# Kernel optimization log

Hardware: AMD Instinct MI355X
Metric: run time of the kernel (lower is better)

Reference implementation:

```python
import jax, jax.numpy as jnp
import numpy as np

HIDDEN = 1024
BATCH = 16
SEQ = 2048
NEG_INF = -1000000000.0


def setup_inputs() -> dict:
    key = jax.random.key(0)
    k1, k2, k3, k4, k5, k6, k7 = jax.random.split(key, 7)
    scale = 1.0 / np.sqrt(HIDDEN)
    return {
        "query": jax.random.normal(k1, (BATCH, HIDDEN), dtype=jnp.float32),
        "keys": jax.random.normal(k2, (BATCH, SEQ, HIDDEN), dtype=jnp.float32),
        "values": jax.random.normal(k3, (BATCH, SEQ, HIDDEN), dtype=jnp.float32),
        "mask": jax.random.randint(k4, (BATCH, SEQ), 0, 2, dtype=jnp.int32),
        # Learned params (nn.Linear(in, out) weight has shape (out, in); we store transposed for x @ W)
        "W1": jax.random.uniform(k5, (HIDDEN, HIDDEN), dtype=jnp.float32, minval=-scale, maxval=scale),
        "W2": jax.random.uniform(k6, (HIDDEN, HIDDEN), dtype=jnp.float32, minval=-scale, maxval=scale),
        "v": jax.random.uniform(k7, (HIDDEN,), dtype=jnp.float32, minval=-scale, maxval=scale),
    }


def reference(query, keys, values, mask, W1, W2, v):
    # scores = v^T tanh(W1 q + W2 k)
    q_proj = query @ W1                       # (b, h)
    k_proj = jnp.einsum('bsh,hd->bsd', keys, W2)  # (b, s, h)
    scores = jnp.einsum('bsh,h->bs', jnp.tanh(q_proj[:, None, :] + k_proj), v)  # (b, s)
    scores = jnp.where(mask == 0, NEG_INF, scores)
    attention_weights = jax.nn.softmax(scores, axis=1)  # (b, s)
    context = jnp.einsum('bs,bsh->bh', attention_weights, values)  # (b, h)
    return context, attention_weights
```

## Files before the change

kernel.cpp:

```cpp
#include <hip/hip_runtime.h>
#include <hip/hip_bf16.h>
#include <cstdint>
#include <cstddef>

#define HIDDEN 1024
#define BATCH 16
#define SEQ 2048
#define M_TOTAL (BATCH*SEQ)
#define NEG_INF -1000000000.0f

typedef unsigned short u16;
typedef __bf16 bf16x8 __attribute__((ext_vector_type(8)));
typedef unsigned short u16x8 __attribute__((ext_vector_type(8)));
typedef unsigned short u16x4 __attribute__((ext_vector_type(4)));
typedef float f32x4 __attribute__((ext_vector_type(4)));

typedef const __attribute__((address_space(1))) void* gas_ptr;
typedef __attribute__((address_space(3))) void* las_ptr;

__device__ __forceinline__ u16 f2bf(float f) {
    unsigned int x = __float_as_uint(f);
    unsigned int r = (x + 0x7fffu + ((x >> 16) & 1u)) >> 16;
    return (u16)r;
}

__device__ __forceinline__ float fast_tanh(float x) {
    float e = __expf(2.0f * x);
    return 1.0f - 2.0f / (e + 1.0f);
}

__global__ __launch_bounds__(256) void qproj_kernel(
    const float* __restrict__ q, const float* __restrict__ W1,
    float* __restrict__ qp)
{
    const int b  = blockIdx.y;
    const int tl = threadIdx.x & 63;
    const int kc = threadIdx.x >> 6;
    const int n  = blockIdx.x * 64 + tl;
    __shared__ float red[4][64];

    const float* qrow = q + b * HIDDEN;
    float acc = 0.f;
    #pragma unroll 8
    for (int k = kc * 256; k < kc * 256 + 256; ++k)
        acc += qrow[k] * W1[(size_t)k * HIDDEN + n];
    red[kc][tl] = acc;
    __syncthreads();
    if (kc == 0)
        qp[b * HIDDEN + n] = red[0][tl] + red[1][tl] + red[2][tl] + red[3][tl];
}

__global__ __launch_bounds__(256) void w2t_kernel(
    const float* __restrict__ W2, u16* __restrict__ W2T)
{
    __shared__ float tile[64][65];
    const int n0 = blockIdx.x * 64, k0 = blockIdx.y * 64;
    const int tid = threadIdx.x;
    const int c = tid & 63, rb = tid >> 6;
    #pragma unroll
    for (int i = 0; i < 16; ++i) {
        int r = rb + i * 4;
        tile[r][c] = W2[(size_t)(k0 + r) * HIDDEN + n0 + c];
    }
    __syncthreads();
    #pragma unroll
    for (int i = 0; i < 16; ++i) {
        int r = rb + i * 4;
        W2T[(size_t)(n0 + r) * HIDDEN + k0 + c] = f2bf(tile[c][r]);
    }
}

__global__ __launch_bounds__(256) void conv_kernel(
    const float* __restrict__ in, u16* __restrict__ out)
{
    int i = blockIdx.x * 256 + threadIdx.x;
    float4 f = ((const float4*)in)[i];
    u16x4 p;
    p[0] = f2bf(f.x); p[1] = f2bf(f.y); p[2] = f2bf(f.z); p[3] = f2bf(f.w);
    ((u16x4*)out)[i] = p;
}

#define BM 128
#define BN 128
#define BK 64

__global__ __launch_bounds__(256) void scores_v2_kernel(
    const u16*   __restrict__ keysb,
    const u16*   __restrict__ W2T,
    const float* __restrict__ qp,
    const float* __restrict__ v,
    float*       __restrict__ part)
{
    __shared__ __align__(16) u16 Alds[BM * BK];
    __shared__ __align__(16) u16 Blds[BN * BK];

    const int tid  = threadIdx.x;
    const int nt   = blockIdx.x;
    const int n0   = nt * BN;
    const int m0   = blockIdx.y * BM;
    const int wave = tid >> 6, lane = tid & 63;
    const int wr = wave >> 1, wc = wave & 1;
    const int quad = lane >> 4, c16 = lane & 15;

    const int sr = tid >> 3;
    const int sc = tid & 7;

    f32x4 acc[4][4];
    #pragma unroll
    for (int i = 0; i < 4; ++i)
        #pragma unroll
        for (int j = 0; j < 4; ++j)
            acc[i][j] = f32x4{0.f, 0.f, 0.f, 0.f};

    for (int kt = 0; kt < HIDDEN; kt += BK) {
        __syncthreads();
        #pragma unroll
        for (int i = 0; i < 4; ++i) {
            int r = sr + i * 32;
            int csw = sc ^ (r & 7);
            const u16* src = keysb + (size_t)(m0 + r) * HIDDEN + kt + csw * 8;
            las_ptr dst = (las_ptr)((char*)Alds + (i * 256 + wave * 64) * 16);
            __builtin_amdgcn_global_load_lds((gas_ptr)src, dst, 16, 0, 0);
        }
        #pragma unroll
        for (int i = 0; i < 4; ++i) {
            int r = sr + i * 32;
            int csw = sc ^ (r & 7);
            const u16* src = W2T + (size_t)(n0 + r) * HIDDEN + kt + csw * 8;
            las_ptr dst = (las_ptr)((char*)Blds + (i * 256 + wave * 64) * 16);
            __builtin_amdgcn_global_load_lds((gas_ptr)src, dst, 16, 0, 0);
        }
        __syncthreads();

        #pragma unroll
        for (int ks = 0; ks < BK; ks += 32) {
            const int ch = (ks >> 3) + quad;
            bf16x8 af[4], bfr[4];
            #pragma unroll
            for (int i = 0; i < 4; ++i) {
                int row = wr * 64 + i * 16 + c16;
                af[i] = __builtin_bit_cast(bf16x8,
                    *(const u16x8*)&Alds[row * BK + ((ch ^ (row & 7)) << 3)]);
            }
            #pragma unroll
            for (int j = 0; j < 4; ++j) {
                int row = wc * 64 + j * 16 + c16;
                bfr[j] = __builtin_bit_cast(bf16x8,
                    *(const u16x8*)&Blds[row * BK + ((ch ^ (row & 7)) << 3)]);
            }
            #pragma unroll
            for (int i = 0; i < 4; ++i)
                #pragma unroll
                for (int j = 0; j < 4; ++j)
                    acc[i][j] = __builtin_amdgcn_mfma_f32_16x16x32_bf16(
                        af[i], bfr[j], acc[i][j], 0, 0, 0);
        }
    }

    const int b = m0 >> 11;
    float qv[4], vv[4];
    #pragma unroll
    for (int j = 0; j < 4; ++j) {
        int n = n0 + wc * 64 + j * 16 + c16;
        qv[j] = qp[b * HIDDEN + n];
        vv[j] = v[n];
    }
    const int slot = nt * 2 + wc;
    #pragma unroll
    for (int i = 0; i < 4; ++i) {
        #pragma unroll
        for (int r = 0; r < 4; ++r) {
            float s = 0.f;
            #pragma unroll
            for (int j = 0; j < 4; ++j)
                s += fast_tanh(acc[i][j][r] + qv[j]) * vv[j];
            s += __shfl_xor(s, 1);
            s += __shfl_xor(s, 2);
            s += __shfl_xor(s, 4);
            s += __shfl_xor(s, 8);
            if (c16 == 0) {
                int m = m0 + wr * 64 + i * 16 + quad * 4 + r;
                part[(size_t)slot * M_TOTAL + m] = s;
            }
        }
    }
}

#define LDA 72

__global__ __launch_bounds__(256) void scores_v1_kernel(
    const float* __restrict__ keys,
    const u16*   __restrict__ W2T,
    const float* __restrict__ qp,
    const float* __restrict__ v,
    float*       __restrict__ part)
{
    __shared__ __align__(16) u16 Alds[BM][LDA];
    __shared__ __align__(16) u16 Blds[BN][LDA];

    const int tid  = threadIdx.x;
    const int nt   = blockIdx.x;
    const int n0   = nt * BN;
    const int m0   = blockIdx.y * BM;
    const int wave = tid >> 6, lane = tid & 63;
    const int wr = wave >> 1, wc = wave & 1;
    const int quad = lane >> 4, c16 = lane & 15;

    f32x4 acc[4][4];
    #pragma unroll
    for (int i = 0; i < 4; ++i)
        #pragma unroll
        for (int j = 0; j < 4; ++j)
            acc[i][j] = f32x4{0.f, 0.f, 0.f, 0.f};

    for (int kt = 0; kt < HIDDEN; kt += BK) {
        __syncthreads();
        const float* gA = keys + (size_t)m0 * HIDDEN + kt;
        #pragma unroll
        for (int i = 0; i < 8; ++i) {
            int idx = tid + i * 256;
            int r = idx >> 4, c4 = idx & 15;
            float4 f = *(const float4*)(gA + (size_t)r * HIDDEN + c4 * 4);
            u16x4 pk;
            pk[0] = f2bf(f.x); pk[1] = f2bf(f.y);
            pk[2] = f2bf(f.z); pk[3] = f2bf(f.w);
            *(u16x4*)&Alds[r][c4 * 4] = pk;
        }
        #pragma unroll
        for (int i = 0; i < 4; ++i) {
            int idx = tid + i * 256;
            int r = idx >> 3, c8 = idx & 7;
            uint4 raw = ((const uint4*)(W2T + (size_t)(n0 + r) * HIDDEN + kt))[c8];
            *(uint4*)&Blds[r][c8 * 8] = raw;
        }
        __syncthreads();

        #pragma unroll
        for (int ks = 0; ks < BK; ks += 32) {
            bf16x8 af[4], bfr[4];
            #pragma unroll
            for (int i = 0; i < 4; ++i)
                af[i] = __builtin_bit_cast(bf16x8,
                    *(const u16x8*)&Alds[wr * 64 + i * 16 + c16][ks + quad * 8]);
            #pragma unroll
            for (int j = 0; j < 4; ++j)
                bfr[j] = __builtin_bit_cast(bf16x8,
                    *(const u16x8*)&Blds[wc * 64 + j * 16 + c16][ks + quad * 8]);
            #pragma unroll
            for (int i = 0; i < 4; ++i)
                #pragma unroll
                for (int j = 0; j < 4; ++j)
                    acc[i][j] = __builtin_amdgcn_mfma_f32_16x16x32_bf16(
                        af[i], bfr[j], acc[i][j], 0, 0, 0);
        }
    }

    const int b = m0 >> 11;
    float qv[4], vv[4];
    #pragma unroll
    for (int j = 0; j < 4; ++j) {
        int n = n0 + wc * 64 + j * 16 + c16;
        qv[j] = qp[b * HIDDEN + n];
        vv[j] = v[n];
    }
    const int slot = nt * 2 + wc;
    #pragma unroll
    for (int i = 0; i < 4; ++i) {
        #pragma unroll
        for (int r = 0; r < 4; ++r) {
            float s = 0.f;
            #pragma unroll
            for (int j = 0; j < 4; ++j)
                s += fast_tanh(acc[i][j][r] + qv[j]) * vv[j];
            s += __shfl_xor(s, 1);
            s += __shfl_xor(s, 2);
            s += __shfl_xor(s, 4);
            s += __shfl_xor(s, 8);
            if (c16 == 0) {
                int m = m0 + wr * 64 + i * 16 + quad * 4 + r;
                part[(size_t)slot * M_TOTAL + m] = s;
            }
        }
    }
}

__global__ __launch_bounds__(1024) void softmax_kernel(
    const float* __restrict__ part, const int* __restrict__ mask,
    float* __restrict__ attn)
{
    const int b = blockIdx.x, tid = threadIdx.x;
    const int wave = tid >> 6, lane = tid & 63;
    __shared__ float red[16];
    float sc[2];
    float mx = -1e30f;
    #pragma unroll
    for (int j = 0; j < 2; ++j) {
        int s = tid + j * 1024;
        float a = 0.f;
        #pragma unroll
        for (int p = 0; p < 16; ++p)
            a += part[(size_t)p * M_TOTAL + b * SEQ + s];
        if (mask[b * SEQ + s] == 0) a = NEG_INF;
        sc[j] = a;
        mx = fmaxf(mx, a);
    }
    #pragma unroll
    for (int o = 32; o > 0; o >>= 1) mx = fmaxf(mx, __shfl_xor(mx, o));
    if (lane == 0) red[wave] = mx;
    __syncthreads();
    #pragma unroll
    for (int w = 0; w < 16; ++w) mx = fmaxf(mx, red[w]);
    float sum = 0.f;
    #pragma unroll
    for (int j = 0; j < 2; ++j) { sc[j] = __expf(sc[j] - mx); sum += sc[j]; }
    #pragma unroll
    for (int o = 32; o > 0; o >>= 1) sum += __shfl_xor(sum, o);
    __syncthreads();
    if (lane == 0) red[wave] = sum;
    __syncthreads();
    sum = 0.f;
    #pragma unroll
    for (int w = 0; w < 16; ++w) sum += red[w];
    float inv = 1.0f / sum;
    #pragma unroll
    for (int j = 0; j < 2; ++j)
        attn[b * SEQ + tid + j * 1024] = sc[j] * inv;
}

__global__ __launch_bounds__(256) void ctx_part_kernel(
    const float* __restrict__ values, const float* __restrict__ attn,
    float* __restrict__ ctxp)
{
    const int b = blockIdx.x, sch = blockIdx.y, tid = threadIdx.x;
    __shared__ float w[32];
    if (tid < 32) w[tid] = attn[b * SEQ + sch * 32 + tid];
    __syncthreads();
    float4 acc = {0.f, 0.f, 0.f, 0.f};
    const float4* V = (const float4*)(values
        + (size_t)b * SEQ * HIDDEN + (size_t)sch * 32 * HIDDEN);
    #pragma unroll 4
    for (int s = 0; s < 32; ++s) {
        float wv = w[s];
        if (wv != 0.0f) {
            float4 x = V[(size_t)s * (HIDDEN / 4) + tid];
            acc.x += wv * x.x; acc.y += wv * x.y;
            acc.z += wv * x.z; acc.w += wv * x.w;
        }
    }
    ((float4*)(ctxp + (size_t)(b * 64 + sch) * HIDDEN))[tid] = acc;
}

__global__ __launch_bounds__(256) void ctx_reduce_kernel(
    const float* __restrict__ ctxp, float* __restrict__ ctx)
{
    const int b = blockIdx.x, tid = threadIdx.x;
    float4 acc = {0.f, 0.f, 0.f, 0.f};
    const float4* P = (const float4*)(ctxp + (size_t)b * 64 * HIDDEN);
    #pragma unroll 8
    for (int s = 0; s < 64; ++s) {
        float4 x = P[(size_t)s * (HIDDEN / 4) + tid];
        acc.x += x.x; acc.y += x.y; acc.z += x.z; acc.w += x.w;
    }
    ((float4*)(ctx + (size_t)b * HIDDEN))[tid] = acc;
}

extern "C" void kernel_launch(void* const* d_in, const int* in_sizes, int n_in,
                              void* d_out, int out_size, void* d_ws, size_t ws_size,
                              hipStream_t stream)
{
    const float* query  = (const float*)d_in[0];
    const float* keys   = (const float*)d_in[1];
    const float* values = (const float*)d_in[2];
    const int*   mask   = (const int*)d_in[3];
    const float* W1     = (const float*)d_in[4];
    const float* W2     = (const float*)d_in[5];
    const float* v      = (const float*)d_in[6];
    float* out = (float*)d_out;

    char* ws = (char*)d_ws;
    float* qp     = (float*)ws;
    u16*   w2t    = (u16*)(ws + (64 << 10));
    float* part   = (float*)(ws + (64 << 10) + (2 << 20));
    float* ctxp   = (float*)(ws + (64 << 10) + (4 << 20));
    u16*   keysb  = (u16*)(ws + (64 << 10) + (8 << 20));
    const size_t WS_BIG = (64 << 10) + (8 << 20) + ((size_t)64 << 20);

    float* attn_out = out + BATCH * HIDDEN;

    qproj_kernel<<<dim3(16, 16), 256, 0, stream>>>(query, W1, qp);
    w2t_kernel  <<<dim3(16, 16), 256, 0, stream>>>(W2, w2t);

    if (ws_size >= WS_BIG) {
        conv_kernel<<<32768, 256, 0, stream>>>(keys, keysb);
        scores_v2_kernel<<<dim3(8, 256), 256, 0, stream>>>(
            keysb, w2t, qp, v, part);
        softmax_kernel<<<16, 1024, 0, stream>>>(part, mask, attn_out);
        ctx_part_kernel<<<dim3(16, 64), 256, 0, stream>>>(
            values, attn_out, ctxp);
        ctx_reduce_kernel<<<16, 256, 0, stream>>>(ctxp, out);
    } else {
        scores_v1_kernel<<<dim3(8, 256), 256, 0, stream>>>(
            keys, w2t, qp, v, part);
        softmax_kernel<<<16, 1024, 0, stream>>>(part, mask, attn_out);
        if (ws_size >= (64 << 10) + (8 << 20)) {
            ctx_part_kernel<<<dim3(16, 64), 256, 0, stream>>>(
                values, attn_out, ctxp);
            ctx_reduce_kernel<<<16, 256, 0, stream>>>(ctxp, out);
        } else {
            hipMemsetAsync(d_out, 0, BATCH * HIDDEN * sizeof(float), stream);
            ctx_part_kernel<<<dim3(16, 64), 256, 0, stream>>>(
                values, attn_out, (float*)d_ws);
            ctx_reduce_kernel<<<16, 256, 0, stream>>>((float*)d_ws, out);
        }
    }
}
```

Before: 413.6 us.

## Fuse prep kernels, reorder scores grid, transpose partial-score layout

Merges keys bf16 conversion, W2 transpose and the query projection into a single launch, cutting two kernel launches and their serialization gaps. The query projection now computes all 16 batches per block, so each W1 element is read once instead of once per batch. The scores grid becomes 1D with the m-tile as the fast index, so consecutive blocks share the same W2T column tile and each key tile is reused across nt. Partial scores are stored m-major so softmax can read 16 partials with four float4 loads. The cost is scattered 4-byte stores in the scores epilogue.

```diff
diff --git a/kernel.cpp b/kernel.cpp
--- a/kernel.cpp
+++ b/kernel.cpp
@@ -29,62 +29,88 @@
     return 1.0f - 2.0f / (e + 1.0f);
 }
 
-__global__ __launch_bounds__(256) void qproj_kernel(
-    const float* __restrict__ q, const float* __restrict__ W1,
-    float* __restrict__ qp)
-{
-    const int b  = blockIdx.y;
-    const int tl = threadIdx.x & 63;
-    const int kc = threadIdx.x >> 6;
-    const int n  = blockIdx.x * 64 + tl;
-    __shared__ float red[4][64];
-
-    const float* qrow = q + b * HIDDEN;
-    float acc = 0.f;
-    #pragma unroll 8
-    for (int k = kc * 256; k < kc * 256 + 256; ++k)
-        acc += qrow[k] * W1[(size_t)k * HIDDEN + n];
-    red[kc][tl] = acc;
+__global__ __launch_bounds__(256) void prep_all_kernel(
+    const float* __restrict__ keys, u16* __restrict__ keysb,
+    const float* __restrict__ W2,   u16* __restrict__ W2T,
+    const float* __restrict__ q,    const float* __restrict__ W1,
+    float* __restrict__ qp, int conv_blocks)
+{
+    __shared__ float lds[64 * 65];
+    int bid = blockIdx.x;
+    const int tid = threadIdx.x;
+
+    if (bid < conv_blocks) {
+        const float4* in4 = (const float4*)keys;
+        u16x4* out4 = (u16x4*)keysb;
+        int base = bid * 1024 + tid;
+        float4 f[4];
+        #pragma unroll
+        for (int i = 0; i < 4; ++i) f[i] = in4[base + i * 256];
+        #pragma unroll
+        for (int i = 0; i < 4; ++i) {
+            u16x4 p;
+            p[0] = f2bf(f[i].x); p[1] = f2bf(f[i].y);
+            p[2] = f2bf(f[i].z); p[3] = f2bf(f[i].w);
+            out4[base + i * 256] = p;
+        }
+        return;
+    }
+    bid -= conv_blocks;
+
+    if (bid < 256) {
+        const int n0 = (bid & 15) * 64, k0 = (bid >> 4) * 64;
+        const int c = tid & 63, rb = tid >> 6;
+        #pragma unroll
+        for (int i = 0; i < 16; ++i) {
+            int r = rb + i * 4;
+            lds[r * 65 + c] = W2[(size_t)(k0 + r) * HIDDEN + n0 + c];
+        }
+        __syncthreads();
+        #pragma unroll
+        for (int i = 0; i < 16; ++i) {
+            int r = rb + i * 4;
+            W2T[(size_t)(n0 + r) * HIDDEN + k0 + c] = f2bf(lds[c * 65 + r]);
+        }
+        return;
+    }
+    bid -= 256;
+
+    const int w = tid >> 6, lane = tid & 63;
+    const int n = bid * 64 + lane;
+    float acc[16];
+    #pragma unroll
+    for (int b = 0; b < 16; ++b) acc[b] = 0.f;
+    const int k0 = w * 256;
+    for (int k = k0; k < k0 + 256; k += 8) {
+        float w1v[8];
+        #pragma unroll
+        for (int u = 0; u < 8; ++u)
+            w1v[u] = W1[(size_t)(k + u) * HIDDEN + n];
+        #pragma unroll
+        for (int u = 0; u < 8; ++u)
+            #pragma unroll
+            for (int b = 0; b < 16; ++b)
+                acc[b] += q[b * HIDDEN + k + u] * w1v[u];
+    }
+    #pragma unroll
+    for (int b = 0; b < 16; ++b)
+        lds[(w * 16 + b) * 64 + lane] = acc[b];
     __syncthreads();
-    if (kc == 0)
-        qp[b * HIDDEN + n] = red[0][tl] + red[1][tl] + red[2][tl] + red[3][tl];
-}
-
-__global__ __launch_bounds__(256) void w2t_kernel(
-    const float* __restrict__ W2, u16* __restrict__ W2T)
-{
-    __shared__ float tile[64][65];
-    const int n0 = blockIdx.x * 64, k0 = blockIdx.y * 64;
-    const int tid = threadIdx.x;
-    const int c = tid & 63, rb = tid >> 6;
-    #pragma unroll
-    for (int i = 0; i < 16; ++i) {
-        int r = rb + i * 4;
-        tile[r][c] = W2[(size_t)(k0 + r) * HIDDEN + n0 + c];
-    }
-    __syncthreads();
-    #pragma unroll
-    for (int i = 0; i < 16; ++i) {
-        int r = rb + i * 4;
-        W2T[(size_t)(n0 + r) * HIDDEN + k0 + c] = f2bf(tile[c][r]);
-    }
-}
-
-__global__ __launch_bounds__(256) void conv_kernel(
-    const float* __restrict__ in, u16* __restrict__ out)
-{
-    int i = blockIdx.x * 256 + threadIdx.x;
-    float4 f = ((const float4*)in)[i];
-    u16x4 p;
-    p[0] = f2bf(f.x); p[1] = f2bf(f.y); p[2] = f2bf(f.z); p[3] = f2bf(f.w);
-    ((u16x4*)out)[i] = p;
+    if (w == 0) {
+        #pragma unroll
+        for (int b = 0; b < 16; ++b) {
+            float s = lds[b * 64 + lane] + lds[(16 + b) * 64 + lane]
+                    + lds[(32 + b) * 64 + lane] + lds[(48 + b) * 64 + lane];
+            qp[b * HIDDEN + n] = s;
+        }
+    }
 }
 
 #define BM 128
 #define BN 128
 #define BK 64
 
-__global__ __launch_bounds__(256) void scores_v2_kernel(
+__global__ __launch_bounds__(256) void scores_v3_kernel(
     const u16*   __restrict__ keysb,
     const u16*   __restrict__ W2T,
     const float* __restrict__ qp,
@@ -95,9 +121,10 @@
     __shared__ __align__(16) u16 Blds[BN * BK];
 
     const int tid  = threadIdx.x;
-    const int nt   = blockIdx.x;
+    const int mt   = blockIdx.x & 255;
+    const int nt   = blockIdx.x >> 8;
+    const int m0   = mt * BM;
     const int n0   = nt * BN;
-    const int m0   = blockIdx.y * BM;
     const int wave = tid >> 6, lane = tid & 63;
     const int wr = wave >> 1, wc = wave & 1;
     const int quad = lane >> 4, c16 = lane & 15;
@@ -180,7 +207,7 @@
             s += __shfl_xor(s, 8);
             if (c16 == 0) {
                 int m = m0 + wr * 64 + i * 16 + quad * 4 + r;
-                part[(size_t)slot * M_TOTAL + m] = s;
+                part[(size_t)m * 16 + slot] = s;
             }
         }
     }
@@ -199,9 +226,10 @@
     __shared__ __align__(16) u16 Blds[BN][LDA];
 
     const int tid  = threadIdx.x;
-    const int nt   = blockIdx.x;
+    const int mt   = blockIdx.x & 255;
+    const int nt   = blockIdx.x >> 8;
+    const int m0   = mt * BM;
     const int n0   = nt * BN;
-    const int m0   = blockIdx.y * BM;
     const int wave = tid >> 6, lane = tid & 63;
     const int wr = wave >> 1, wc = wave & 1;
     const int quad = lane >> 4, c16 = lane & 15;
@@ -278,7 +306,7 @@
             s += __shfl_xor(s, 8);
             if (c16 == 0) {
                 int m = m0 + wr * 64 + i * 16 + quad * 4 + r;
-                part[(size_t)slot * M_TOTAL + m] = s;
+                part[(size_t)m * 16 + slot] = s;
             }
         }
     }
@@ -296,10 +324,10 @@
     #pragma unroll
     for (int j = 0; j < 2; ++j) {
         int s = tid + j * 1024;
-        float a = 0.f;
-        #pragma unroll
-        for (int p = 0; p < 16; ++p)
-            a += part[(size_t)p * M_TOTAL + b * SEQ + s];
+        const float4* p4 = (const float4*)(part + ((size_t)(b * SEQ + s) << 4));
+        float4 a0 = p4[0], a1 = p4[1], a2 = p4[2], a3 = p4[3];
+        float a = (a0.x + a0.y + a0.z + a0.w) + (a1.x + a1.y + a1.z + a1.w)
+                + (a2.x + a2.y + a2.z + a2.w) + (a3.x + a3.y + a3.z + a3.w);
         if (mask[b * SEQ + s] == 0) a = NEG_INF;
         sc[j] = a;
         mx = fmaxf(mx, a);
@@ -387,20 +415,18 @@
 
     float* attn_out = out + BATCH * HIDDEN;
 
-    qproj_kernel<<<dim3(16, 16), 256, 0, stream>>>(query, W1, qp);
-    w2t_kernel  <<<dim3(16, 16), 256, 0, stream>>>(W2, w2t);
-
     if (ws_size >= WS_BIG) {
-        conv_kernel<<<32768, 256, 0, stream>>>(keys, keysb);
-        scores_v2_kernel<<<dim3(8, 256), 256, 0, stream>>>(
-            keysb, w2t, qp, v, part);
+        prep_all_kernel<<<8192 + 256 + 16, 256, 0, stream>>>(
+            keys, keysb, W2, w2t, query, W1, qp, 8192);
+        scores_v3_kernel<<<2048, 256, 0, stream>>>(keysb, w2t, qp, v, part);
         softmax_kernel<<<16, 1024, 0, stream>>>(part, mask, attn_out);
         ctx_part_kernel<<<dim3(16, 64), 256, 0, stream>>>(
             values, attn_out, ctxp);
         ctx_reduce_kernel<<<16, 256, 0, stream>>>(ctxp, out);
     } else {
-        scores_v1_kernel<<<dim3(8, 256), 256, 0, stream>>>(
-            keys, w2t, qp, v, part);
+        prep_all_kernel<<<256 + 16, 256, 0, stream>>>(
+            keys, keysb, W2, w2t, query, W1, qp, 0);
+        scores_v1_kernel<<<2048, 256, 0, stream>>>(keys, w2t, qp, v, part);
         softmax_kernel<<<16, 1024, 0, stream>>>(part, mask, attn_out);
         if (ws_size >= (64 << 10) + (8 << 20)) {
             ctx_part_kernel<<<dim3(16, 64), 256, 0, stream>>>(
```

After: 435.1 us. 5.2% more time.
